# Optimization experiments

Measured on AMD Instinct MI355X. Metric: run time of the kernel, lower is better.

Reference implementation:

```python
import jax, jax.numpy as jnp
import numpy as np

B, V, N, C, H = 4, 8, 256, 768, 12
DH = C // H
NEG = -1e9


def setup_inputs() -> dict:
    key = jax.random.key(0)
    k0, k1, k2, k3, k4, k5 = jax.random.split(key, 6)
    feats = jax.random.normal(k0, (B, V, N, C), dtype=jnp.float32)
    is_ref = jax.random.randint(k1, (B, V), 0, 2).astype(bool)
    # nn.MultiheadAttention params: packed in_proj (3C, C) + bias, out_proj Linear(C, C)
    w_qkv = jax.random.normal(k2, (3 * C, C), dtype=jnp.float32) * 0.02
    b_qkv = jax.random.normal(k3, (3 * C,), dtype=jnp.float32) * 0.02
    w_out = jax.random.normal(k4, (C, C), dtype=jnp.float32) * 0.02
    b_out = jax.random.normal(k5, (C,), dtype=jnp.float32) * 0.02
    return {"feats": feats, "is_ref": is_ref, "w_qkv": w_qkv, "b_qkv": b_qkv,
            "w_out": w_out, "b_out": b_out}


def reference(feats, is_ref, w_qkv, b_qkv, w_out, b_out):
    b_, v_, n_, c_ = feats.shape
    # packed QKV projection (torch Linear: x @ W.T + b)
    qkv = feats @ w_qkv.T + b_qkv                      # (B,V,N,3C)
    q, k, v = jnp.split(qkv, 3, axis=-1)
    q = q.reshape(b_, v_, n_, H, DH) * (1.0 / jnp.sqrt(jnp.float32(DH)))
    k = k.reshape(b_, v_ * n_, H, DH)                  # keys flattened over views
    v = v.reshape(b_, v_ * n_, H, DH)
    # view v attends to views w with opposite ref flag
    allowed = is_ref[:, :, None] ^ is_ref[:, None, :]  # (B,V,V) bool
    key_mask = jnp.repeat(allowed, n_, axis=2)         # (B,V,V*N)
    scores = jnp.einsum('bvnhd,bmhd->bhvnm', q, k)     # (B,H,V,N,V*N)
    logits = jnp.where(key_mask[:, None, :, None, :], scores, NEG)
    attn = jax.nn.softmax(logits, axis=-1)
    ctx = jnp.einsum('bhvnm,bmhd->bvnhd', attn, v).reshape(b_, v_, n_, c_)
    out = ctx @ w_out.T + b_out
    # views with empty context pass through unchanged
    has_ctx = allowed.any(axis=-1)                     # (B,V)
    return jnp.where(has_ctx[:, :, None, None], out, feats)
```

## Files before the change

kernel.cpp:

```cpp
#include <hip/hip_runtime.h>
#include <hip/hip_bf16.h>
#include <math.h>

#define BDIM 4
#define VDIM 8
#define NDIM 256
#define CDIM 768
#define HDIM 12
#define DHE  64
#define C3   (3*CDIM)
#define ROWS (BDIM*VDIM*NDIM)
#define KEYS (VDIM*NDIM)

typedef __attribute__((ext_vector_type(8))) short short8;
typedef __attribute__((ext_vector_type(4))) float float4v;

__device__ inline unsigned short f2bf(float f) {
    unsigned int u = __builtin_bit_cast(unsigned int, f);
    u += 0x7fffu + ((u >> 16) & 1u);
    return (unsigned short)(u >> 16);
}

__device__ __forceinline__ unsigned int pk2(float a, float b) {
    return (unsigned int)f2bf(a) | ((unsigned int)f2bf(b) << 16);
}

__device__ __forceinline__ uint4 pk8(float4 a, float4 b) {
    uint4 r;
    r.x = pk2(a.x, a.y); r.y = pk2(a.z, a.w);
    r.z = pk2(b.x, b.y); r.w = pk2(b.z, b.w);
    return r;
}

__device__ __forceinline__ void gld_lds16(const unsigned short* g, unsigned short* l) {
    __builtin_amdgcn_global_load_lds(
        (const __attribute__((address_space(1))) void*)g,
        (__attribute__((address_space(3))) void*)l, 16, 0, 0);
}

#define NA8 786432
#define NW8 221184
#define NO8 73728

__global__ __launch_bounds__(256) void cast_bf16_all(
    const float* __restrict__ fA, const float* __restrict__ fW,
    const float* __restrict__ fO,
    unsigned short* __restrict__ bA, unsigned short* __restrict__ bW,
    unsigned short* __restrict__ bO)
{
    const int gid = blockIdx.x * 256 + threadIdx.x;
    const float* src;
    unsigned short* dst;
    int idx;
    if (gid < NA8)            { src = fA; dst = bA; idx = gid; }
    else if (gid < NA8 + NW8) { src = fW; dst = bW; idx = gid - NA8; }
    else                      { src = fO; dst = bO; idx = gid - NA8 - NW8; }
    const float4* p = (const float4*)(src + (size_t)idx * 8);
    *(uint4*)(dst + (size_t)idx * 8) = pk8(p[0], p[1]);
}

__global__ __launch_bounds__(256) void gemm_qkv_mfma(
    const unsigned short* __restrict__ A,
    const unsigned short* __restrict__ W,
    const float* __restrict__ bias,
    unsigned short* __restrict__ out,
    unsigned short* __restrict__ vT)
{
    __shared__ __attribute__((aligned(16))) unsigned short As[128][32];
    __shared__ __attribute__((aligned(16))) unsigned short Ws[128][32];
    const int t = threadIdx.x;
    const int wave = t >> 6, lane = t & 63;
    const int m = lane & 15, quad = lane >> 4;
    const int wr = (wave >> 1) * 64, wc = (wave & 1) * 64;
    const int row0 = blockIdx.y * 128, col0 = blockIdx.x * 128;

    const int sr = t >> 2, sk = (t & 3) * 8;
    const unsigned short* ag = &A[(size_t)(row0 + sr) * CDIM + sk];
    const unsigned short* wg = &W[(size_t)(col0 + sr) * CDIM + sk];
    unsigned short* la0 = &As[sr][sk];
    unsigned short* la1 = &As[64 + sr][sk];
    unsigned short* lw0 = &Ws[sr][sk];
    unsigned short* lw1 = &Ws[64 + sr][sk];

    float4v acc[4][4] = {};

    for (int k0 = 0; k0 < CDIM; k0 += 32) {
        gld_lds16(ag + k0, la0);
        gld_lds16(ag + (size_t)64 * CDIM + k0, la1);
        gld_lds16(wg + k0, lw0);
        gld_lds16(wg + (size_t)64 * CDIM + k0, lw1);
        __syncthreads();
        short8 a[4], b[4];
        #pragma unroll
        for (int rt = 0; rt < 4; rt++)
            a[rt] = *(const short8*)&As[wr + rt * 16 + m][quad * 8];
        #pragma unroll
        for (int ct = 0; ct < 4; ct++)
            b[ct] = *(const short8*)&Ws[wc + ct * 16 + m][quad * 8];
        #pragma unroll
        for (int rt = 0; rt < 4; rt++)
            #pragma unroll
            for (int ct = 0; ct < 4; ct++)
                acc[rt][ct] = __builtin_amdgcn_mfma_f32_16x16x32_bf16(
                    a[rt], b[ct], acc[rt][ct], 0, 0, 0);
        __syncthreads();
    }

    if (col0 < 2 * CDIM) {
        #pragma unroll
        for (int ct = 0; ct < 4; ct++) {
            const int col = col0 + wc + ct * 16 + m;
            const float bv = bias[col];
            #pragma unroll
            for (int rt = 0; rt < 4; rt++) {
                const size_t row = (size_t)row0 + wr + rt * 16 + quad * 4;
                #pragma unroll
                for (int r = 0; r < 4; r++)
                    out[(row + r) * C3 + col] = f2bf(acc[rt][ct][r] + bv);
            }
        }
    } else {
        #pragma unroll
        for (int ct = 0; ct < 4; ct++) {
            const int vcol = col0 + wc + ct * 16 + m - 2 * CDIM;
            const int h = vcol >> 6, d = vcol & 63;
            const float bv = bias[col0 + wc + ct * 16 + m];
            #pragma unroll
            for (int rt = 0; rt < 4; rt++) {
                const int row = row0 + wr + rt * 16 + quad * 4;
                const int bidx = row >> 11, key = row & 2047;
                ushort4 pkv;
                pkv.x = f2bf(acc[rt][ct][0] + bv);
                pkv.y = f2bf(acc[rt][ct][1] + bv);
                pkv.z = f2bf(acc[rt][ct][2] + bv);
                pkv.w = f2bf(acc[rt][ct][3] + bv);
                *(ushort4*)&vT[((size_t)(bidx * HDIM + h) * DHE + d) * KEYS + key] = pkv;
            }
        }
    }
}

__global__ __launch_bounds__(256, 3) void attn_mfma(
    const unsigned short* __restrict__ qkv,
    const unsigned short* __restrict__ vT,
    const int* __restrict__ is_ref,
    unsigned short* __restrict__ ctx)
{
    const int gid = blockIdx.x;
    const int grp = gid % 48;
    const int sub = gid / 48;
    const int b = grp / HDIM, h = grp % HDIM;
    const int v = sub & 7, half = sub >> 3;

    const int t = threadIdx.x, wave = t >> 6, lane = t & 63;
    const int m = lane & 15, quad = lane >> 4;
    const int n0 = half * 128 + wave * 32;

    __shared__ unsigned short Ks[128][64];
    __shared__ unsigned short Vs[64][128];
    __shared__ unsigned short Ps[4][32][72];

    const int my_ref = is_ref[b * VDIM + v];
    unsigned amask = 0;
    #pragma unroll
    for (int w = 0; w < VDIM; w++)
        if ((is_ref[b * VDIM + w] != 0) ^ (my_ref != 0)) amask |= 1u << w;
    const int nChunks = 2 * __popc(amask);

    const float c1 = 0.18033688f;

    short8 aq[2][2];
    #pragma unroll
    for (int qt = 0; qt < 2; qt++) {
        const size_t row = (size_t)((b * VDIM + v) * NDIM) + n0 + qt * 16 + m;
        #pragma unroll
        for (int ks = 0; ks < 2; ks++)
            aq[qt][ks] = *(const short8*)&qkv[row * C3 + h * DHE + ks * 32 + quad * 8];
    }

    float rs[2] = {0.f, 0.f};
    float4v O[2][4] = {};

    const int k_key = t >> 3, k_dg = t & 7;
    const int v_dim = t >> 4, v_kg = t & 15;

    const unsigned short* vTb = vT + (size_t)(b * HDIM + h) * DHE * KEYS;

    uint4 kreg[4], vreg[4];
    unsigned rem = amask;
    int wcur = __builtin_ffs((int)rem) - 1;

    if (nChunks > 0) {
        const unsigned short* kb =
            qkv + (size_t)((b * VDIM + wcur) * NDIM) * C3 + CDIM + h * DHE;
        #pragma unroll
        for (int i = 0; i < 4; i++)
            kreg[i] = *(const uint4*)&kb[(size_t)(i * 32 + k_key) * C3 + k_dg * 8];
        #pragma unroll
        for (int i = 0; i < 4; i++)
            vreg[i] = *(const uint4*)&vTb[(size_t)(i * 16 + v_dim) * KEYS
                                          + wcur * NDIM + v_kg * 8];
    }

    for (int ci = 0; ci < nChunks; ci++) {
        __syncthreads();
        #pragma unroll
        for (int i = 0; i < 4; i++)
            *(uint4*)&Ks[i * 32 + k_key][(k_dg ^ (k_key & 7)) * 8] = kreg[i];
        #pragma unroll
        for (int i = 0; i < 4; i++)
            *(uint4*)&Vs[i * 16 + v_dim][(v_kg ^ v_dim) * 8] = vreg[i];

        if (ci + 1 < nChunks) {
            int wn, m0n;
            if ((ci & 1) == 0) { wn = wcur; m0n = 128; }
            else {
                unsigned r2 = rem & (rem - 1);
                wn = __builtin_ffs((int)r2) - 1; m0n = 0;
            }
            const unsigned short* kb =
                qkv + (size_t)((b * VDIM + wn) * NDIM + m0n) * C3 + CDIM + h * DHE;
            #pragma unroll
            for (int i = 0; i < 4; i++)
                kreg[i] = *(const uint4*)&kb[(size_t)(i * 32 + k_key) * C3 + k_dg * 8];
            #pragma unroll
            for (int i = 0; i < 4; i++)
                vreg[i] = *(const uint4*)&vTb[(size_t)(i * 16 + v_dim) * KEYS
                                              + wn * NDIM + m0n + v_kg * 8];
        }
        __syncthreads();

        #pragma unroll
        for (int hk = 0; hk < 2; hk++) {
            #pragma unroll
            for (int kt = 0; kt < 4; kt++) {
                const int nt = hk * 4 + kt;
                const short8 bk0 = *(const short8*)&Ks[nt * 16 + m][(quad ^ (m & 7)) * 8];
                const short8 bk1 = *(const short8*)&Ks[nt * 16 + m][((4 + quad) ^ (m & 7)) * 8];
                #pragma unroll
                for (int qt = 0; qt < 2; qt++) {
                    float4v s = {};
                    s = __builtin_amdgcn_mfma_f32_16x16x32_bf16(bk0, aq[qt][0], s, 0, 0, 0);
                    s = __builtin_amdgcn_mfma_f32_16x16x32_bf16(bk1, aq[qt][1], s, 0, 0, 0);
                    const float p0 = __builtin_amdgcn_exp2f(s[0] * c1);
                    const float p1 = __builtin_amdgcn_exp2f(s[1] * c1);
                    const float p2 = __builtin_amdgcn_exp2f(s[2] * c1);
                    const float p3 = __builtin_amdgcn_exp2f(s[3] * c1);
                    rs[qt] += (p0 + p1) + (p2 + p3);
                    uint2 pw;
                    pw.x = pk2(p0, p1);
                    pw.y = pk2(p2, p3);
                    *(uint2*)&Ps[wave][qt * 16 + m][kt * 16 + quad * 4] = pw;
                }
            }
            #pragma unroll
            for (int kk = 0; kk < 2; kk++) {
                const short8 ap0 = *(const short8*)&Ps[wave][m][kk * 32 + quad * 8];
                const short8 ap1 = *(const short8*)&Ps[wave][16 + m][kk * 32 + quad * 8];
                #pragma unroll
                for (int ct = 0; ct < 4; ct++) {
                    const short8 bv = *(const short8*)&Vs[ct * 16 + m]
                        [((hk * 8 + kk * 4 + quad) ^ m) * 8];
                    O[0][ct] = __builtin_amdgcn_mfma_f32_16x16x32_bf16(ap0, bv, O[0][ct], 0, 0, 0);
                    O[1][ct] = __builtin_amdgcn_mfma_f32_16x16x32_bf16(ap1, bv, O[1][ct], 0, 0, 0);
                }
            }
        }
        if (ci & 1) { rem &= rem - 1; wcur = __builtin_ffs((int)rem) - 1; }
    }

    #pragma unroll
    for (int qt = 0; qt < 2; qt++) {
        float x = rs[qt];
        x += __shfl_xor(x, 16, 64);
        x += __shfl_xor(x, 32, 64);
        const float inv = (x > 0.f) ? 1.f / x : 0.f;
        float invq[4];
        #pragma unroll
        for (int r = 0; r < 4; r++)
            invq[r] = __shfl(inv, quad * 4 + r, 64);
        const size_t rowg = (size_t)((b * VDIM + v) * NDIM) + n0 + qt * 16 + quad * 4;
        #pragma unroll
        for (int ct = 0; ct < 4; ct++)
            #pragma unroll
            for (int r = 0; r < 4; r++)
                ctx[(rowg + r) * CDIM + h * DHE + ct * 16 + m] = f2bf(O[qt][ct][r] * invq[r]);
    }
}

__global__ __launch_bounds__(256) void gemm_out_mfma(
    const unsigned short* __restrict__ A,
    const unsigned short* __restrict__ W,
    const float* __restrict__ bias,
    const float* __restrict__ feats,
    const int* __restrict__ is_ref,
    float* __restrict__ out)
{
    __shared__ __attribute__((aligned(16))) unsigned short As[128][32];
    __shared__ __attribute__((aligned(16))) unsigned short Ws[128][32];
    const int t = threadIdx.x;
    const int wave = t >> 6, lane = t & 63;
    const int m = lane & 15, quad = lane >> 4;
    const int wr = (wave >> 1) * 64, wc = (wave & 1) * 64;
    const int row0 = blockIdx.y * 128, col0 = blockIdx.x * 128;

    const int sr = t >> 2, sk = (t & 3) * 8;
    const unsigned short* ag = &A[(size_t)(row0 + sr) * CDIM + sk];
    const unsigned short* wg = &W[(size_t)(col0 + sr) * CDIM + sk];
    unsigned short* la0 = &As[sr][sk];
    unsigned short* la1 = &As[64 + sr][sk];
    unsigned short* lw0 = &Ws[sr][sk];
    unsigned short* lw1 = &Ws[64 + sr][sk];

    float4v acc[4][4] = {};

    for (int k0 = 0; k0 < CDIM; k0 += 32) {
        gld_lds16(ag + k0, la0);
        gld_lds16(ag + (size_t)64 * CDIM + k0, la1);
        gld_lds16(wg + k0, lw0);
        gld_lds16(wg + (size_t)64 * CDIM + k0, lw1);
        __syncthreads();
        short8 a[4], b[4];
        #pragma unroll
        for (int rt = 0; rt < 4; rt++)
            a[rt] = *(const short8*)&As[wr + rt * 16 + m][quad * 8];
        #pragma unroll
        for (int ct = 0; ct < 4; ct++)
            b[ct] = *(const short8*)&Ws[wc + ct * 16 + m][quad * 8];
        #pragma unroll
        for (int rt = 0; rt < 4; rt++)
            #pragma unroll
            for (int ct = 0; ct < 4; ct++)
                acc[rt][ct] = __builtin_amdgcn_mfma_f32_16x16x32_bf16(
                    a[rt], b[ct], acc[rt][ct], 0, 0, 0);
        __syncthreads();
    }

    const int bidx = row0 / (VDIM * NDIM);
    const int vidx = (row0 / NDIM) % VDIM;
    const int my = is_ref[bidx * VDIM + vidx];
    bool has = false;
    #pragma unroll
    for (int w = 0; w < VDIM; w++) has = has || (is_ref[bidx * VDIM + w] != my);

    #pragma unroll
    for (int ct = 0; ct < 4; ct++) {
        const int col = col0 + wc + ct * 16 + m;
        const float bv = bias[col];
        #pragma unroll
        for (int rt = 0; rt < 4; rt++) {
            const size_t row = (size_t)row0 + wr + rt * 16 + quad * 4;
            #pragma unroll
            for (int r = 0; r < 4; r++) {
                float o = acc[rt][ct][r] + bv;
                if (!has) o = feats[(row + r) * CDIM + col];
                out[(row + r) * CDIM + col] = o;
            }
        }
    }
}

extern "C" void kernel_launch(void* const* d_in, const int* in_sizes, int n_in,
                              void* d_out, int out_size, void* d_ws, size_t ws_size,
                              hipStream_t stream) {
    const float* feats = (const float*)d_in[0];
    const int*   is_ref = (const int*)d_in[1];
    const float* w_qkv = (const float*)d_in[2];
    const float* b_qkv = (const float*)d_in[3];
    const float* w_out = (const float*)d_in[4];
    const float* b_out = (const float*)d_in[5];
    float* out = (float*)d_out;

    unsigned short* qkv_b = (unsigned short*)d_ws;
    unsigned short* vT    = qkv_b + (size_t)ROWS * C3;
    unsigned short* ctx_b = vT + (size_t)BDIM * HDIM * DHE * KEYS;
    unsigned short* A_bf  = ctx_b + (size_t)ROWS * CDIM;
    unsigned short* Wq_bf = A_bf + (size_t)ROWS * CDIM;
    unsigned short* Wo_bf = Wq_bf + (size_t)C3 * CDIM;

    cast_bf16_all<<<dim3((NA8 + NW8 + NO8) / 256), 256, 0, stream>>>(
        feats, w_qkv, w_out, A_bf, Wq_bf, Wo_bf);

    dim3 g1(C3 / 128, ROWS / 128);
    gemm_qkv_mfma<<<g1, 256, 0, stream>>>(A_bf, Wq_bf, b_qkv, qkv_b, vT);

    attn_mfma<<<dim3(768), 256, 0, stream>>>(qkv_b, vT, is_ref, ctx_b);

    dim3 g3(CDIM / 128, ROWS / 128);
    gemm_out_mfma<<<g3, 256, 0, stream>>>(ctx_b, Wo_bf, b_out, feats, is_ref, out);
    (void)in_sizes; (void)n_in; (void)out_size; (void)ws_size;
}
```

Measured before the change: 255.8 us.

## Split attention into smaller query tiles and read V directly from global

Each block now covers 64 query rows (16 per wave) instead of 128, doubling the grid to 1536 blocks, and the launch bound targets 4 blocks per SM. The V shared-memory tile and its register prefetch are removed, so each wave reads V fragments straight from global/L2 in the PV MFMA loop. This cuts LDS and register use to raise occupancy and parallelism. The cost is that K is loaded twice as often across blocks, V reads are no longer staged or shared within a block, and the PV loop now waits on global-memory latency.

```diff
diff --git a/kernel.cpp b/kernel.cpp
--- a/kernel.cpp
+++ b/kernel.cpp
@@ -140,7 +140,7 @@
     }
 }
 
-__global__ __launch_bounds__(256, 3) void attn_mfma(
+__global__ __launch_bounds__(256, 4) void attn_mfma(
     const unsigned short* __restrict__ qkv,
     const unsigned short* __restrict__ vT,
     const int* __restrict__ is_ref,
@@ -150,15 +150,14 @@
     const int grp = gid % 48;
     const int sub = gid / 48;
     const int b = grp / HDIM, h = grp % HDIM;
-    const int v = sub & 7, half = sub >> 3;
+    const int v = sub & 7, q4 = sub >> 3;
 
     const int t = threadIdx.x, wave = t >> 6, lane = t & 63;
     const int m = lane & 15, quad = lane >> 4;
-    const int n0 = half * 128 + wave * 32;
+    const int n0 = q4 * 64 + wave * 16;
 
     __shared__ unsigned short Ks[128][64];
-    __shared__ unsigned short Vs[64][128];
-    __shared__ unsigned short Ps[4][32][72];
+    __shared__ unsigned short Ps[4][16][72];
 
     const int my_ref = is_ref[b * VDIM + v];
     unsigned amask = 0;
@@ -169,24 +168,22 @@
 
     const float c1 = 0.18033688f;
 
-    short8 aq[2][2];
-    #pragma unroll
-    for (int qt = 0; qt < 2; qt++) {
-        const size_t row = (size_t)((b * VDIM + v) * NDIM) + n0 + qt * 16 + m;
+    short8 aq[2];
+    {
+        const size_t row = (size_t)((b * VDIM + v) * NDIM) + n0 + m;
         #pragma unroll
         for (int ks = 0; ks < 2; ks++)
-            aq[qt][ks] = *(const short8*)&qkv[row * C3 + h * DHE + ks * 32 + quad * 8];
-    }
-
-    float rs[2] = {0.f, 0.f};
-    float4v O[2][4] = {};
+            aq[ks] = *(const short8*)&qkv[row * C3 + h * DHE + ks * 32 + quad * 8];
+    }
+
+    float rs = 0.f;
+    float4v O[4] = {};
 
     const int k_key = t >> 3, k_dg = t & 7;
-    const int v_dim = t >> 4, v_kg = t & 15;
 
     const unsigned short* vTb = vT + (size_t)(b * HDIM + h) * DHE * KEYS;
 
-    uint4 kreg[4], vreg[4];
+    uint4 kreg[4];
     unsigned rem = amask;
     int wcur = __builtin_ffs((int)rem) - 1;
 
@@ -196,20 +193,14 @@
         #pragma unroll
         for (int i = 0; i < 4; i++)
             kreg[i] = *(const uint4*)&kb[(size_t)(i * 32 + k_key) * C3 + k_dg * 8];
-        #pragma unroll
-        for (int i = 0; i < 4; i++)
-            vreg[i] = *(const uint4*)&vTb[(size_t)(i * 16 + v_dim) * KEYS
-                                          + wcur * NDIM + v_kg * 8];
     }
 
     for (int ci = 0; ci < nChunks; ci++) {
+        const int base = wcur * NDIM + (ci & 1) * 128;
         __syncthreads();
         #pragma unroll
         for (int i = 0; i < 4; i++)
             *(uint4*)&Ks[i * 32 + k_key][(k_dg ^ (k_key & 7)) * 8] = kreg[i];
-        #pragma unroll
-        for (int i = 0; i < 4; i++)
-            *(uint4*)&Vs[i * 16 + v_dim][(v_kg ^ v_dim) * 8] = vreg[i];
 
         if (ci + 1 < nChunks) {
             int wn, m0n;
@@ -223,10 +214,6 @@
             #pragma unroll
             for (int i = 0; i < 4; i++)
                 kreg[i] = *(const uint4*)&kb[(size_t)(i * 32 + k_key) * C3 + k_dg * 8];
-            #pragma unroll
-            for (int i = 0; i < 4; i++)
-                vreg[i] = *(const uint4*)&vTb[(size_t)(i * 16 + v_dim) * KEYS
-                                              + wn * NDIM + m0n + v_kg * 8];
         }
         __syncthreads();
 
@@ -237,41 +224,35 @@
                 const int nt = hk * 4 + kt;
                 const short8 bk0 = *(const short8*)&Ks[nt * 16 + m][(quad ^ (m & 7)) * 8];
                 const short8 bk1 = *(const short8*)&Ks[nt * 16 + m][((4 + quad) ^ (m & 7)) * 8];
-                #pragma unroll
-                for (int qt = 0; qt < 2; qt++) {
-                    float4v s = {};
-                    s = __builtin_amdgcn_mfma_f32_16x16x32_bf16(bk0, aq[qt][0], s, 0, 0, 0);
-                    s = __builtin_amdgcn_mfma_f32_16x16x32_bf16(bk1, aq[qt][1], s, 0, 0, 0);
-                    const float p0 = __builtin_amdgcn_exp2f(s[0] * c1);
-                    const float p1 = __builtin_amdgcn_exp2f(s[1] * c1);
-                    const float p2 = __builtin_amdgcn_exp2f(s[2] * c1);
-                    const float p3 = __builtin_amdgcn_exp2f(s[3] * c1);
-                    rs[qt] += (p0 + p1) + (p2 + p3);
-                    uint2 pw;
-                    pw.x = pk2(p0, p1);
-                    pw.y = pk2(p2, p3);
-                    *(uint2*)&Ps[wave][qt * 16 + m][kt * 16 + quad * 4] = pw;
-                }
+                float4v s = {};
+                s = __builtin_amdgcn_mfma_f32_16x16x32_bf16(bk0, aq[0], s, 0, 0, 0);
+                s = __builtin_amdgcn_mfma_f32_16x16x32_bf16(bk1, aq[1], s, 0, 0, 0);
+                const float p0 = __builtin_amdgcn_exp2f(s[0] * c1);
+                const float p1 = __builtin_amdgcn_exp2f(s[1] * c1);
+                const float p2 = __builtin_amdgcn_exp2f(s[2] * c1);
+                const float p3 = __builtin_amdgcn_exp2f(s[3] * c1);
+                rs += (p0 + p1) + (p2 + p3);
+                uint2 pw;
+                pw.x = pk2(p0, p1);
+                pw.y = pk2(p2, p3);
+                *(uint2*)&Ps[wave][m][kt * 16 + quad * 4] = pw;
             }
             #pragma unroll
             for (int kk = 0; kk < 2; kk++) {
-                const short8 ap0 = *(const short8*)&Ps[wave][m][kk * 32 + quad * 8];
-                const short8 ap1 = *(const short8*)&Ps[wave][16 + m][kk * 32 + quad * 8];
+                const short8 ap = *(const short8*)&Ps[wave][m][kk * 32 + quad * 8];
                 #pragma unroll
                 for (int ct = 0; ct < 4; ct++) {
-                    const short8 bv = *(const short8*)&Vs[ct * 16 + m]
-                        [((hk * 8 + kk * 4 + quad) ^ m) * 8];
-                    O[0][ct] = __builtin_amdgcn_mfma_f32_16x16x32_bf16(ap0, bv, O[0][ct], 0, 0, 0);
-                    O[1][ct] = __builtin_amdgcn_mfma_f32_16x16x32_bf16(ap1, bv, O[1][ct], 0, 0, 0);
+                    const short8 bv = *(const short8*)&vTb[
+                        (size_t)(ct * 16 + m) * KEYS + base + hk * 64 + kk * 32 + quad * 8];
+                    O[ct] = __builtin_amdgcn_mfma_f32_16x16x32_bf16(ap, bv, O[ct], 0, 0, 0);
                 }
             }
         }
         if (ci & 1) { rem &= rem - 1; wcur = __builtin_ffs((int)rem) - 1; }
     }
 
-    #pragma unroll
-    for (int qt = 0; qt < 2; qt++) {
-        float x = rs[qt];
+    {
+        float x = rs;
         x += __shfl_xor(x, 16, 64);
         x += __shfl_xor(x, 32, 64);
         const float inv = (x > 0.f) ? 1.f / x : 0.f;
@@ -279,12 +260,12 @@
         #pragma unroll
         for (int r = 0; r < 4; r++)
             invq[r] = __shfl(inv, quad * 4 + r, 64);
-        const size_t rowg = (size_t)((b * VDIM + v) * NDIM) + n0 + qt * 16 + quad * 4;
+        const size_t rowg = (size_t)((b * VDIM + v) * NDIM) + n0 + quad * 4;
         #pragma unroll
         for (int ct = 0; ct < 4; ct++)
             #pragma unroll
             for (int r = 0; r < 4; r++)
-                ctx[(rowg + r) * CDIM + h * DHE + ct * 16 + m] = f2bf(O[qt][ct][r] * invq[r]);
+                ctx[(rowg + r) * CDIM + h * DHE + ct * 16 + m] = f2bf(O[ct][r] * invq[r]);
     }
 }
 
@@ -384,7 +365,7 @@
     dim3 g1(C3 / 128, ROWS / 128);
     gemm_qkv_mfma<<<g1, 256, 0, stream>>>(A_bf, Wq_bf, b_qkv, qkv_b, vT);
 
-    attn_mfma<<<dim3(768), 256, 0, stream>>>(qkv_b, vT, is_ref, ctx_b);
+    attn_mfma<<<dim3(1536), 256, 0, stream>>>(qkv_b, vT, is_ref, ctx_b);
 
     dim3 g3(CDIM / 128, ROWS / 128);
     gemm_out_mfma<<<g3, 256, 0, stream>>>(ctx_b, Wo_bf, b_out, feats, is_ref, out);
```

Result: slower. 328.4 us (+28.4%).

## Schedule attention blocks longest-first with serpentine ordering across CUs

Applied to the files above, without the earlier changes.

Adds a small single-block kernel that computes each attention task's workload (number of allowed views) from is_ref and builds a permutation sorting tasks by descending length. The attention kernel maps blockIdx through this permutation, reversing order on alternate 256-block rounds, to balance load across compute units. It adds an extra kernel launch with serial O(n^2) ranking work, and the load balance depends on how blocks are actually dispatched to CUs.

```diff
diff --git a/kernel.cpp b/kernel.cpp
--- a/kernel.cpp
+++ b/kernel.cpp
@@ -59,6 +59,42 @@
     *(uint4*)(dst + (size_t)idx * 8) = pk8(p[0], p[1]);
 }
 
+__global__ __launch_bounds__(256) void sched_tasks(
+    const int* __restrict__ is_ref, int* __restrict__ perm)
+{
+    __shared__ unsigned char lenS[768];
+    __shared__ int base[9];
+    const int t = threadIdx.x;
+    for (int i = t; i < 768; i += 256) {
+        const int grp = i >> 4, sub = i & 15;
+        const int b = grp / HDIM, v = sub & 7;
+        const int my = is_ref[b * VDIM + v];
+        int cnt = 0;
+        #pragma unroll
+        for (int w = 0; w < VDIM; w++)
+            if ((is_ref[b * VDIM + w] != 0) != (my != 0)) cnt++;
+        lenS[i] = (unsigned char)cnt;
+    }
+    __syncthreads();
+    if (t < 9) {
+        int c = 0;
+        for (int i = 0; i < 768; i++) if (lenS[i] == t) c++;
+        base[t] = c;
+    }
+    __syncthreads();
+    if (t == 0) {
+        int acc = 0;
+        for (int j = 8; j >= 0; j--) { int c = base[j]; base[j] = acc; acc += c; }
+    }
+    __syncthreads();
+    for (int i = t; i < 768; i += 256) {
+        const int L = lenS[i];
+        int rank = 0;
+        for (int k = 0; k < i; k++) rank += (lenS[k] == L);
+        perm[base[L] + rank] = i;
+    }
+}
+
 __global__ __launch_bounds__(256) void gemm_qkv_mfma(
     const unsigned short* __restrict__ A,
     const unsigned short* __restrict__ W,
@@ -144,11 +180,15 @@
     const unsigned short* __restrict__ qkv,
     const unsigned short* __restrict__ vT,
     const int* __restrict__ is_ref,
-    unsigned short* __restrict__ ctx)
+    unsigned short* __restrict__ ctx,
+    const int* __restrict__ perm)
 {
-    const int gid = blockIdx.x;
-    const int grp = gid % 48;
-    const int sub = gid / 48;
+    const int g = blockIdx.x;
+    const int round = g >> 8, cu = g & 255;
+    const int idx = (round & 1) ? ((round << 8) | (255 - cu)) : g;
+    const int task = perm[idx];
+    const int grp = task >> 4;
+    const int sub = task & 15;
     const int b = grp / HDIM, h = grp % HDIM;
     const int v = sub & 7, half = sub >> 3;
 
@@ -377,6 +417,9 @@
     unsigned short* A_bf  = ctx_b + (size_t)ROWS * CDIM;
     unsigned short* Wq_bf = A_bf + (size_t)ROWS * CDIM;
     unsigned short* Wo_bf = Wq_bf + (size_t)C3 * CDIM;
+    int* perm = (int*)(Wo_bf + (size_t)CDIM * CDIM);
+
+    sched_tasks<<<dim3(1), 256, 0, stream>>>(is_ref, perm);
 
     cast_bf16_all<<<dim3((NA8 + NW8 + NO8) / 256), 256, 0, stream>>>(
         feats, w_qkv, w_out, A_bf, Wq_bf, Wo_bf);
@@ -384,7 +427,7 @@
     dim3 g1(C3 / 128, ROWS / 128);
     gemm_qkv_mfma<<<g1, 256, 0, stream>>>(A_bf, Wq_bf, b_qkv, qkv_b, vT);
 
-    attn_mfma<<<dim3(768), 256, 0, stream>>>(qkv_b, vT, is_ref, ctx_b);
+    attn_mfma<<<dim3(768), 256, 0, stream>>>(qkv_b, vT, is_ref, ctx_b, perm);
 
     dim3 g3(CDIM / 128, ROWS / 128);
     gemm_out_mfma<<<g3, 256, 0, stream>>>(ctx_b, Wo_bf, b_out, feats, is_ref, out);
```

Result: slower. 305.9 us (+19.6%).
